# Performance work log

Measured on AMD Instinct MI355X. Metric: run time of the kernel, lower is better.

## Reference

```python
import jax, jax.numpy as jnp
import numpy as np
import math

IN_FEATURES = 4096
OUT_FEATURES = 4096
TOKENS = 8192


def hydrate_weight(seed, out_features, in_features):
    """Deterministically synthesize the virtual weight matrix from the 64-bit seed.
    Mirrors nn.Linear's kaiming-uniform-style bound (1/sqrt(fan_in)) used by gmem_rs
    hydration; never stored as a parameter."""
    bound = 1.0 / math.sqrt(in_features)
    key = jax.random.key(seed)
    return jax.random.uniform(
        key, (out_features, in_features), dtype=jnp.float32,
        minval=-bound, maxval=bound)


def setup_inputs() -> dict:
    key = jax.random.key(0)
    kx, kb = jax.random.split(key)
    x = jax.random.normal(kx, (TOKENS, IN_FEATURES), dtype=jnp.float32)
    bound = 1.0 / math.sqrt(IN_FEATURES)
    bias = jax.random.uniform(kb, (OUT_FEATURES,), dtype=jnp.float32,
                              minval=-bound, maxval=bound)
    return {"x": x, "bias": bias, "seed": 1140071481}


def reference(x, bias, seed):
    # Hydrate weight on-the-fly from seed (zero-RAM virtual weight), then GEMM.
    W = hydrate_weight(seed, OUT_FEATURES, IN_FEATURES)  # [out, in]
    y = jnp.einsum('ti,oi->to', x, W)  # [tokens, out]
    return y + bias
```

## Files before the change

kernel.cpp:

```cpp
#include <hip/hip_runtime.h>
#include <hip/hip_bf16.h>
#include <stdint.h>

#define TOKENS 8192
#define NOUT   4096
#define KIN    4096

#define BM 256
#define BN 256
#define BK 64
#define NT (KIN / BK)

typedef __attribute__((ext_vector_type(8))) short bf16x8;
typedef __attribute__((ext_vector_type(4))) float f32x4;

__device__ __forceinline__ uint32_t rotl32(uint32_t x, int r) {
  return (x << r) | (x >> (32 - r));
}

__device__ __forceinline__ uint16_t f2bf_rne(float f) {
  uint32_t u = __float_as_uint(f);
  u += 0x7FFFu + ((u >> 16) & 1u);
  return (uint16_t)(u >> 16);
}

__device__ __forceinline__ void threefry2x32(uint32_t k0, uint32_t k1,
                                             uint32_t c0, uint32_t c1,
                                             uint32_t& o0, uint32_t& o1) {
  uint32_t ks2 = 0x1BD11BDAu ^ k0 ^ k1;
  uint32_t x0 = c0 + k0;
  uint32_t x1 = c1 + k1;
#define TFR(r) { x0 += x1; x1 = rotl32(x1, (r)); x1 ^= x0; }
  TFR(13) TFR(15) TFR(26) TFR(6)
  x0 += k1;  x1 += ks2 + 1u;
  TFR(17) TFR(29) TFR(16) TFR(24)
  x0 += ks2; x1 += k0 + 2u;
  TFR(13) TFR(15) TFR(26) TFR(6)
  x0 += k0;  x1 += k1 + 3u;
  TFR(17) TFR(29) TFR(16) TFR(24)
  x0 += k1;  x1 += ks2 + 4u;
  TFR(13) TFR(15) TFR(26) TFR(6)
  x0 += ks2; x1 += k0 + 5u;
#undef TFR
  o0 = x0; o1 = x1;
}

__global__ void prep_kernel(const float* __restrict__ x,
                            uint16_t* __restrict__ xb,
                            uint16_t* __restrict__ W,
                            const int* __restrict__ seed_ptr) {
  uint32_t b = blockIdx.x;
  uint32_t g = b / 5u, r = b % 5u;
  if (r < 4u) {
    uint32_t k1 = (uint32_t)(*seed_ptr);
    uint32_t j = (g * 4u + r) * 256u + threadIdx.x;
    uint32_t o0, o1;
    threefry2x32(0u, k1, 0u, j, o0, o1);
    uint32_t bits = o0 ^ o1;
    const float scale = 0.03125f;
    const float mn    = -0.015625f;
    float f = __uint_as_float((bits >> 9) | 0x3F800000u) - 1.0f;
    float v = fmaxf(mn, f * scale + mn);
    W[j] = f2bf_rne(v);
  } else {
    uint32_t base = (g * 256u + threadIdx.x) * 8u;
    f32x4 a = *(const f32x4*)(x + base);
    f32x4 c = *(const f32x4*)(x + base + 4);
    union { uint16_t u[8]; bf16x8 v; } rr;
    rr.u[0] = f2bf_rne(a[0]); rr.u[1] = f2bf_rne(a[1]);
    rr.u[2] = f2bf_rne(a[2]); rr.u[3] = f2bf_rne(a[3]);
    rr.u[4] = f2bf_rne(c[0]); rr.u[5] = f2bf_rne(c[1]);
    rr.u[6] = f2bf_rne(c[2]); rr.u[7] = f2bf_rne(c[3]);
    *(bf16x8*)(xb + base) = rr.v;
  }
}

__global__ __launch_bounds__(512, 2)
void gemm_bias_kernel(const uint16_t* __restrict__ A,
                      const uint16_t* __restrict__ B,
                      const float* __restrict__ bias,
                      float* __restrict__ C) {
  __shared__ uint16_t smem[2][2][16384];

  const int nwgn = NOUT / BN;
  const int nwg  = (TOKENS / BM) * nwgn;
  int bid = blockIdx.x;
  int cpx = nwg >> 3;
  int swzb = (bid & 7) * cpx + (bid >> 3);
  int tm = (swzb / nwgn) * BM;
  int tn = (swzb % nwgn) * BN;

  const int t    = threadIdx.x;
  const int lane = t & 63;
  const int wid  = t >> 6;
  const int wm   = wid >> 2;
  const int wn   = wid & 3;
  const int fr   = lane & 15;
  const int fq   = lane >> 4;

  const int swzRd = (lane & 7) << 4;
  const int lsw   = ((lane & 7) ^ (lane >> 3)) << 4;

  const char* sA  = (const char*)(A + (size_t)(tm + wid * 16 + (lane >> 3)) * KIN) + lsw;
  const char* sB  = (const char*)(B + (size_t)(tn + wid * 16 + (lane >> 3)) * KIN) + lsw;
  const char* sA1 = sA + (size_t)128 * KIN * 2;
  const char* sB1 = sB + (size_t)128 * KIN * 2;

  char* const dstB = (char*)&smem[0][0][0] + wid * 2048 + lane * 16;

  f32x4 acc[8][4] = {};
  bf16x8 af[2][4], bv0[2][2], bv1[2][2];

  auto stage2 = [&](const char* src, char* dst) {
    __builtin_amdgcn_global_load_lds(
        (const __attribute__((address_space(1))) void*)src,
        (__attribute__((address_space(3))) void*)dst, 16, 0, 0);
    __builtin_amdgcn_global_load_lds(
        (const __attribute__((address_space(1))) void*)(src + (size_t)8 * KIN * 2),
        (__attribute__((address_space(3))) void*)(dst + 1024), 16, 0, 0);
  };

#define VMW(N) asm volatile("s_waitcnt vmcnt(" #N ")" ::: "memory")
#define LKW(N) asm volatile("s_waitcnt lgkmcnt(" #N ")" ::: "memory")
#define SB0    __builtin_amdgcn_sched_barrier(0)
#define PRI(p) __builtin_amdgcn_s_setprio(p)

#define RD_AS(BUFI, MH, S)                                                     \
    _Pragma("unroll")                                                          \
    for (int i_ = 0; i_ < 4; ++i_)                                             \
      af[S][i_] = *(const bf16x8*)((const char*)&smem[BUFI][0][0] +            \
          (wm * 64 + (MH) * 128 + i_ * 16 + fr) * 128 +                        \
          ((((S) << 6) | (fq << 4)) ^ swzRd));

#define RD_BS(BUFI, BV, NH, S)                                                 \
    _Pragma("unroll")                                                          \
    for (int j_ = 0; j_ < 2; ++j_)                                             \
      BV[S][j_] = *(const bf16x8*)((const char*)&smem[BUFI][1][0] +            \
          (wn * 32 + (NH) * 128 + j_ * 16 + fr) * 128 +                        \
          ((((S) << 6) | (fq << 4)) ^ swzRd));

#define MF8(MH, NH, BV, S)                                                     \
    _Pragma("unroll")                                                          \
    for (int i_ = 0; i_ < 4; ++i_)                                             \
      _Pragma("unroll")                                                        \
      for (int j_ = 0; j_ < 2; ++j_)                                           \
        acc[(MH) * 4 + i_][(NH) * 2 + j_] =                                    \
            __builtin_amdgcn_mfma_f32_16x16x32_bf16(                           \
                af[S][i_], BV[S][j_], acc[(MH) * 4 + i_][(NH) * 2 + j_],       \
                0, 0, 0);

#define KTILE(BUF, OFF1, OFF2, MODE)                                           \
  {                                                                            \
                                                            \
    __builtin_amdgcn_s_barrier();                                              \
    if ((MODE) <= 1) stage2(sA1 + (OFF1),                                      \
                            dstB + ((BUF) ^ 1) * 65536 + 16384);               \
    RD_AS(BUF, 0, 0) RD_BS(BUF, bv0, 0, 0)                                     \
    SB0;                                                                       \
    RD_AS(BUF, 0, 1) RD_BS(BUF, bv0, 0, 1)                                     \
    SB0;                                                                       \
    RD_BS(BUF, bv1, 1, 0) RD_BS(BUF, bv1, 1, 1)                                \
    LKW(10); SB0; PRI(1); MF8(0, 0, bv0, 0)                                    \
    LKW(4);  SB0; MF8(0, 0, bv0, 1)                                            \
    LKW(0);  SB0; MF8(0, 1, bv1, 0) MF8(0, 1, bv1, 1) PRI(0);                  \
                                                            \
    RD_AS(BUF, 1, 0)                                                           \
    SB0;                                                                       \
    RD_AS(BUF, 1, 1)                                                           \
    __builtin_amdgcn_s_barrier();                                              \
    if ((MODE) == 0) {                                                         \
      stage2(sA  + (OFF2), dstB + (BUF) * 65536);                              \
      stage2(sB  + (OFF2), dstB + (BUF) * 65536 + 32768);                      \
      stage2(sB1 + (OFF2), dstB + (BUF) * 65536 + 49152);                      \
    }                                                                          \
    LKW(4); SB0; PRI(1); MF8(1, 0, bv0, 0)                                     \
    LKW(0); SB0; MF8(1, 0, bv0, 1) MF8(1, 1, bv1, 0) MF8(1, 1, bv1, 1) PRI(0); \
    if ((MODE) == 0) { VMW(6); } else if ((MODE) == 1) { VMW(0); }             \
  }

  stage2(sA,        dstB);
  stage2(sB,        dstB + 32768);
  stage2(sB1,       dstB + 49152);
  stage2(sA1,       dstB + 16384);
  stage2(sA  + 128, dstB + 65536);
  stage2(sB  + 128, dstB + 65536 + 32768);
  stage2(sB1 + 128, dstB + 65536 + 49152);
  VMW(6);

  for (int it = 0; it < (NT - 2) / 2; ++it) {
    KTILE(0, 128, 256, 0)
    KTILE(1, 256, 384, 0)
    sA += 256; sB += 256; sA1 += 256; sB1 += 256;
  }
  KTILE(0, 128, 0, 1)
  KTILE(1, 0, 0, 2)

#undef KTILE
#undef MF8
#undef RD_BS
#undef RD_AS
#undef PRI
#undef SB0
#undef LKW
#undef VMW

#pragma unroll
  for (int nj = 0; nj < 4; ++nj) {
    const int nh = nj >> 1, j = nj & 1;
    const int col = tn + wn * 32 + nh * 128 + j * 16 + fr;
    const float bvs = bias[col];
#pragma unroll
    for (int mi = 0; mi < 8; ++mi) {
      const int mh = mi >> 2, i = mi & 3;
      const int row0 = tm + wm * 64 + mh * 128 + i * 16 + fq * 4;
#pragma unroll
      for (int rr = 0; rr < 4; ++rr)
        C[(size_t)(row0 + rr) * NOUT + col] = acc[mi][nj][rr] + bvs;
    }
  }
}

extern "C" void kernel_launch(void* const* d_in, const int* in_sizes, int n_in,
                              void* d_out, int out_size, void* d_ws, size_t ws_size,
                              hipStream_t stream) {
  const float* x    = (const float*)d_in[0];
  const float* bias = (const float*)d_in[1];
  const int*   seed = (const int*)d_in[2];
  float* y = (float*)d_out;

  uint16_t* Wb = (uint16_t*)d_ws;
  uint16_t* Xb = Wb + (size_t)NOUT * KIN;

  prep_kernel<<<81920, 256, 0, stream>>>(x, Xb, Wb, seed);

  const int grid = (TOKENS / BM) * (NOUT / BN);
  gemm_bias_kernel<<<grid, 512, 0, stream>>>(Xb, Wb, bias, y);
}
```

Baseline: 259.2 us.

## Restructure K-loop to single-barrier prefetch with even/odd wave-staggered MFMA order

```diff
diff --git a/kernel.cpp b/kernel.cpp
--- a/kernel.cpp
+++ b/kernel.cpp
@@ -97,6 +97,7 @@
   const int wn   = wid & 3;
   const int fr   = lane & 15;
   const int fq   = lane >> 4;
+  const bool evenW = (wid & 1) == 0;
 
   const int swzRd = (lane & 7) << 4;
   const int lsw   = ((lane & 7) ^ (lane >> 3)) << 4;
@@ -149,51 +150,79 @@
                 af[S][i_], BV[S][j_], acc[(MH) * 4 + i_][(NH) * 2 + j_],       \
                 0, 0, 0);
 
-#define KTILE(BUF, OFF1, OFF2, MODE)                                           \
+#define KTILE(BUF, OFF, MODE)                                                  \
   {                                                                            \
-                                                            \
-    __builtin_amdgcn_s_barrier();                                              \
-    if ((MODE) <= 1) stage2(sA1 + (OFF1),                                      \
-                            dstB + ((BUF) ^ 1) * 65536 + 16384);               \
-    RD_AS(BUF, 0, 0) RD_BS(BUF, bv0, 0, 0)                                     \
-    SB0;                                                                       \
-    RD_AS(BUF, 0, 1) RD_BS(BUF, bv0, 0, 1)                                     \
-    SB0;                                                                       \
-    RD_BS(BUF, bv1, 1, 0) RD_BS(BUF, bv1, 1, 1)                                \
-    LKW(10); SB0; PRI(1); MF8(0, 0, bv0, 0)                                    \
-    LKW(4);  SB0; MF8(0, 0, bv0, 1)                                            \
-    LKW(0);  SB0; MF8(0, 1, bv1, 0) MF8(0, 1, bv1, 1) PRI(0);                  \
-                                                            \
-    RD_AS(BUF, 1, 0)                                                           \
-    SB0;                                                                       \
-    RD_AS(BUF, 1, 1)                                                           \
+    VMW(0);                                                                    \
     __builtin_amdgcn_s_barrier();                                              \
     if ((MODE) == 0) {                                                         \
-      stage2(sA  + (OFF2), dstB + (BUF) * 65536);                              \
-      stage2(sB  + (OFF2), dstB + (BUF) * 65536 + 32768);                      \
-      stage2(sB1 + (OFF2), dstB + (BUF) * 65536 + 49152);                      \
+      stage2(sA  + (OFF), dstB + ((BUF) ^ 1) * 65536);                         \
+      stage2(sB  + (OFF), dstB + ((BUF) ^ 1) * 65536 + 32768);                 \
+      stage2(sA1 + (OFF), dstB + ((BUF) ^ 1) * 65536 + 16384);                 \
+      stage2(sB1 + (OFF), dstB + ((BUF) ^ 1) * 65536 + 49152);                 \
     }                                                                          \
-    LKW(4); SB0; PRI(1); MF8(1, 0, bv0, 0)                                     \
-    LKW(0); SB0; MF8(1, 0, bv0, 1) MF8(1, 1, bv1, 0) MF8(1, 1, bv1, 1) PRI(0); \
-    if ((MODE) == 0) { VMW(6); } else if ((MODE) == 1) { VMW(0); }             \
-  }
-
-  stage2(sA,        dstB);
-  stage2(sB,        dstB + 32768);
-  stage2(sB1,       dstB + 49152);
-  stage2(sA1,       dstB + 16384);
-  stage2(sA  + 128, dstB + 65536);
-  stage2(sB  + 128, dstB + 65536 + 32768);
-  stage2(sB1 + 128, dstB + 65536 + 49152);
-  VMW(6);
+    if (evenW) {                                                               \
+                                                                      \
+      RD_AS(BUF, 0, 0) RD_BS(BUF, bv0, 0, 0)                                   \
+      SB0;                                                                     \
+      RD_AS(BUF, 0, 1) RD_BS(BUF, bv0, 0, 1)                                   \
+      SB0;                                                                     \
+      LKW(6); SB0; PRI(1); MF8(0, 0, bv0, 0)                                   \
+      LKW(0); SB0; MF8(0, 0, bv0, 1) PRI(0);                                   \
+                                                                      \
+      RD_BS(BUF, bv1, 1, 0)                                                    \
+      SB0;                                                                     \
+      RD_BS(BUF, bv1, 1, 1)                                                    \
+      SB0;                                                                     \
+      LKW(2); SB0; PRI(1); MF8(0, 1, bv1, 0)                                   \
+      LKW(0); SB0; MF8(0, 1, bv1, 1) PRI(0);                                   \
+                                                                      \
+      RD_AS(BUF, 1, 0)                                                         \
+      SB0;                                                                     \
+      RD_AS(BUF, 1, 1)                                                         \
+      SB0;                                                                     \
+      LKW(4); SB0; PRI(1); MF8(1, 1, bv1, 0)                                   \
+      LKW(0); SB0; MF8(1, 1, bv1, 1) PRI(0);                                   \
+                                                               \
+      PRI(1); MF8(1, 0, bv0, 0) MF8(1, 0, bv0, 1) PRI(0);                      \
+    } else {                                                                   \
+                                                                      \
+      RD_AS(BUF, 1, 0) RD_BS(BUF, bv1, 1, 0)                                   \
+      SB0;                                                                     \
+      RD_AS(BUF, 1, 1) RD_BS(BUF, bv1, 1, 1)                                   \
+      SB0;                                                                     \
+      LKW(6); SB0; PRI(1); MF8(1, 1, bv1, 0)                                   \
+      LKW(0); SB0; MF8(1, 1, bv1, 1) PRI(0);                                   \
+                                                                      \
+      RD_BS(BUF, bv0, 0, 0)                                                    \
+      SB0;                                                                     \
+      RD_BS(BUF, bv0, 0, 1)                                                    \
+      SB0;                                                                     \
+      LKW(2); SB0; PRI(1); MF8(1, 0, bv0, 0)                                   \
+      LKW(0); SB0; MF8(1, 0, bv0, 1) PRI(0);                                   \
+                                                                      \
+      RD_AS(BUF, 0, 0)                                                         \
+      SB0;                                                                     \
+      RD_AS(BUF, 0, 1)                                                         \
+      SB0;                                                                     \
+      LKW(4); SB0; PRI(1); MF8(0, 0, bv0, 0)                                   \
+      LKW(0); SB0; MF8(0, 0, bv0, 1) PRI(0);                                   \
+                                                               \
+      PRI(1); MF8(0, 1, bv1, 0) MF8(0, 1, bv1, 1) PRI(0);                      \
+    }                                                                          \
+  }
+
+  stage2(sA,  dstB);
+  stage2(sB,  dstB + 32768);
+  stage2(sA1, dstB + 16384);
+  stage2(sB1, dstB + 49152);
 
   for (int it = 0; it < (NT - 2) / 2; ++it) {
-    KTILE(0, 128, 256, 0)
-    KTILE(1, 256, 384, 0)
+    KTILE(0, 128, 0)
+    KTILE(1, 256, 0)
     sA += 256; sB += 256; sA1 += 256; sB1 += 256;
   }
-  KTILE(0, 128, 0, 1)
-  KTILE(1, 0, 0, 2)
+  KTILE(0, 128, 0)
+  KTILE(1, 0, 1)
 
 #undef KTILE
 #undef MF8
```

Result: slower. 810.6 us (+212.7%).

## Restructure K-tile into four barrier-separated phases with precomputed LDS offsets

Applied to the files above, without the earlier changes.

```diff
diff --git a/kernel.cpp b/kernel.cpp
--- a/kernel.cpp
+++ b/kernel.cpp
@@ -87,8 +87,8 @@
   int bid = blockIdx.x;
   int cpx = nwg >> 3;
   int swzb = (bid & 7) * cpx + (bid >> 3);
-  int tm = (swzb / nwgn) * BM;
-  int tn = (swzb % nwgn) * BN;
+  const int tm = (swzb / nwgn) * BM;
+  const int tn = (swzb % nwgn) * BN;
 
   const int t    = threadIdx.x;
   const int lane = t & 63;
@@ -106,7 +106,17 @@
   const char* sA1 = sA + (size_t)128 * KIN * 2;
   const char* sB1 = sB + (size_t)128 * KIN * 2;
 
-  char* const dstB = (char*)&smem[0][0][0] + wid * 2048 + lane * 16;
+  char* const smemB = (char*)&smem[0][0][0];
+  char* const dstB  = smemB + wid * 2048 + lane * 16;
+
+  const int rA00 = (wm * 64 + fr) * 128 + ((fq << 4) ^ swzRd);
+  const int rA01 = rA00 ^ 64;
+  const int rA10 = rA00 + 65536;
+  const int rA11 = rA10 ^ 64;
+  const int rB00 = 32768 + (wn * 32 + fr) * 128 + ((fq << 4) ^ swzRd);
+  const int rB01 = rB00 ^ 64;
+  const int rB10 = rB00 + 65536;
+  const int rB11 = rB10 ^ 64;
 
   f32x4 acc[8][4] = {};
   bf16x8 af[2][4], bv0[2][2], bv1[2][2];
@@ -125,19 +135,15 @@
 #define SB0    __builtin_amdgcn_sched_barrier(0)
 #define PRI(p) __builtin_amdgcn_s_setprio(p)
 
-#define RD_AS(BUFI, MH, S)                                                     \
+#define RD_A4(BASE, S)                                                         \
     _Pragma("unroll")                                                          \
     for (int i_ = 0; i_ < 4; ++i_)                                             \
-      af[S][i_] = *(const bf16x8*)((const char*)&smem[BUFI][0][0] +            \
-          (wm * 64 + (MH) * 128 + i_ * 16 + fr) * 128 +                        \
-          ((((S) << 6) | (fq << 4)) ^ swzRd));
-
-#define RD_BS(BUFI, BV, NH, S)                                                 \
+      af[S][i_] = *(const bf16x8*)(smemB + (BASE) + i_ * 2048);
+
+#define RD_B2(BASE, BV, S)                                                     \
     _Pragma("unroll")                                                          \
     for (int j_ = 0; j_ < 2; ++j_)                                             \
-      BV[S][j_] = *(const bf16x8*)((const char*)&smem[BUFI][1][0] +            \
-          (wn * 32 + (NH) * 128 + j_ * 16 + fr) * 128 +                        \
-          ((((S) << 6) | (fq << 4)) ^ swzRd));
+      BV[S][j_] = *(const bf16x8*)(smemB + (BASE) + j_ * 2048);
 
 #define MF8(MH, NH, BV, S)                                                     \
     _Pragma("unroll")                                                          \
@@ -151,41 +157,47 @@
 
 #define KTILE(BUF, OFF1, OFF2, MODE)                                           \
   {                                                                            \
-                                                            \
-    __builtin_amdgcn_s_barrier();                                              \
+                       \
+    RD_A4((BUF) ? rA10 : rA00, 0) RD_B2((BUF) ? rB10 : rB00, bv0, 0)           \
+    SB0;                                                                       \
+    RD_A4((BUF) ? rA11 : rA01, 1) RD_B2((BUF) ? rB11 : rB01, bv0, 1)           \
     if ((MODE) <= 1) stage2(sA1 + (OFF1),                                      \
                             dstB + ((BUF) ^ 1) * 65536 + 16384);               \
-    RD_AS(BUF, 0, 0) RD_BS(BUF, bv0, 0, 0)                                     \
+    __builtin_amdgcn_s_barrier();                                              \
+    LKW(6); SB0; PRI(1); MF8(0, 0, bv0, 0)                                     \
+    LKW(0); SB0; MF8(0, 0, bv0, 1) PRI(0);                                     \
+                                                   \
+    RD_B2(((BUF) ? rB10 : rB00) + 16384, bv1, 0)                               \
     SB0;                                                                       \
-    RD_AS(BUF, 0, 1) RD_BS(BUF, bv0, 0, 1)                                     \
+    RD_B2(((BUF) ? rB11 : rB01) + 16384, bv1, 1)                               \
+    __builtin_amdgcn_s_barrier();                                              \
+    LKW(2); SB0; PRI(1); MF8(0, 1, bv1, 0)                                     \
+    LKW(0); SB0; MF8(0, 1, bv1, 1) PRI(0);                                     \
+            \
+    RD_A4(((BUF) ? rA10 : rA00) + 16384, 0)                                    \
     SB0;                                                                       \
-    RD_BS(BUF, bv1, 1, 0) RD_BS(BUF, bv1, 1, 1)                                \
-    LKW(10); SB0; PRI(1); MF8(0, 0, bv0, 0)                                    \
-    LKW(4);  SB0; MF8(0, 0, bv0, 1)                                            \
-    LKW(0);  SB0; MF8(0, 1, bv1, 0) MF8(0, 1, bv1, 1) PRI(0);                  \
-                                                            \
-    RD_AS(BUF, 1, 0)                                                           \
-    SB0;                                                                       \
-    RD_AS(BUF, 1, 1)                                                           \
-    __builtin_amdgcn_s_barrier();                                              \
-    if ((MODE) == 0) {                                                         \
-      stage2(sA  + (OFF2), dstB + (BUF) * 65536);                              \
-      stage2(sB  + (OFF2), dstB + (BUF) * 65536 + 32768);                      \
-      stage2(sB1 + (OFF2), dstB + (BUF) * 65536 + 49152);                      \
-    }                                                                          \
-    LKW(4); SB0; PRI(1); MF8(1, 0, bv0, 0)                                     \
-    LKW(0); SB0; MF8(1, 0, bv0, 1) MF8(1, 1, bv1, 0) MF8(1, 1, bv1, 1) PRI(0); \
+    RD_A4(((BUF) ? rA11 : rA01) + 16384, 1)                                    \
+    if ((MODE) == 0) { stage2(sA + (OFF2), dstB + (BUF) * 65536);              \
+                       stage2(sB + (OFF2), dstB + (BUF) * 65536 + 32768); }    \
+    __builtin_amdgcn_s_barrier();                                              \
+    LKW(4); SB0; PRI(1); MF8(1, 1, bv1, 0)                                     \
+    LKW(0); SB0; MF8(1, 1, bv1, 1) PRI(0);                                     \
+        \
+    if ((MODE) == 0) stage2(sB1 + (OFF2), dstB + (BUF) * 65536 + 49152);       \
     if ((MODE) == 0) { VMW(6); } else if ((MODE) == 1) { VMW(0); }             \
+    __builtin_amdgcn_s_barrier();                                              \
+    SB0; PRI(1); MF8(1, 0, bv0, 0) MF8(1, 0, bv0, 1) PRI(0);                   \
   }
 
   stage2(sA,        dstB);
   stage2(sB,        dstB + 32768);
+  stage2(sA1,       dstB + 16384);
   stage2(sB1,       dstB + 49152);
-  stage2(sA1,       dstB + 16384);
   stage2(sA  + 128, dstB + 65536);
   stage2(sB  + 128, dstB + 65536 + 32768);
   stage2(sB1 + 128, dstB + 65536 + 49152);
   VMW(6);
+  __builtin_amdgcn_s_barrier();
 
   for (int it = 0; it < (NT - 2) / 2; ++it) {
     KTILE(0, 128, 256, 0)
@@ -197,8 +209,8 @@
 
 #undef KTILE
 #undef MF8
-#undef RD_BS
-#undef RD_AS
+#undef RD_B2
+#undef RD_A4
 #undef PRI
 #undef SB0
 #undef LKW
```

New measurement: 251.1 us. -3.1%, faster.
